# Performance work log

Hardware: AMD Instinct MI355X
Metric: run time of the kernel (lower is better)

Reference implementation:

```python
import jax, jax.numpy as jnp
import numpy as np

B, E, T, H = 4, 16, 1024, 1024
NEG = -10000.0


def setup_inputs() -> dict:
    key = jax.random.key(0)
    ks = jax.random.split(key, 9)
    s = 1.0 / np.sqrt(H)
    return {
        "token_embedding": jax.random.normal(ks[0], (B, T, H), jnp.float32),
        "entity_embedding": jax.random.normal(ks[1], (B, E, H), jnp.float32),
        "token_mask": jax.random.bernoulli(ks[2], 0.9, (B, T)),
        "Wt": jax.random.normal(ks[3], (H, H), jnp.float32) * s,
        "bt": jax.random.normal(ks[4], (H,), jnp.float32) * s,
        "We": jax.random.normal(ks[5], (H, H), jnp.float32) * s,
        "be": jax.random.normal(ks[6], (H,), jnp.float32) * s,
        "Wp": jax.random.normal(ks[7], (H,), jnp.float32) * s,
        "bp": jax.random.normal(ks[8], (1,), jnp.float32) * s,
    }


def reference(token_embedding, entity_embedding, token_mask, Wt, bt, We, be, Wp, bp):
    # token branch: [B,T,H] @ [H,H] -> [B,T,H]
    t = jnp.einsum('bth,hk->btk', token_embedding, Wt) + bt
    # entity branch: [B,E,H] @ [H,H] -> [B,E,H]
    e = jnp.einsum('beh,hk->bek', entity_embedding, We) + be
    # broadcast add -> relu -> linear-to-scalar: [B,E,T,H] -> [B,E,T]
    m = jax.nn.relu(t[:, None, :, :] + e[:, :, None, :])
    cls = jnp.einsum('beth,h->bet', m, Wp) + bp[0]
    # mask fill (after squeeze, per squeeze=True path)
    cls = jnp.where(token_mask[:, None, :], cls, NEG)
    p = jax.nn.sigmoid(cls)
    return cls, p
```

## Files before the change

kernel.cpp:

```cpp
#include <hip/hip_runtime.h>

typedef unsigned short us;
typedef __attribute__((ext_vector_type(8))) short short8;
typedef __attribute__((ext_vector_type(4))) float f32x4;

__device__ __forceinline__ us f2bf(float f) {
  unsigned int u = __builtin_bit_cast(unsigned int, f);
  u += 0x7fffu + ((u >> 16) & 1u);
  return (us)(u >> 16);
}

__device__ __forceinline__ void gload_lds16(const void* g, void* l) {
  __builtin_amdgcn_global_load_lds(
      (const __attribute__((address_space(1))) void*)g,
      (__attribute__((address_space(3))) void*)l, 16, 0, 0);
}

__global__ __launch_bounds__(256) void prep_kernel(
    const float* __restrict__ token, us* __restrict__ tokb,
    const float* __restrict__ Wt, us* __restrict__ WtT,
    const float* __restrict__ entity, const float* __restrict__ We,
    float* __restrict__ epart) {
  __shared__ float tile[64][65];
  __shared__ float eS[16][128];
  const int bid = blockIdx.x, tid = threadIdx.x;
  if (bid < 256) {
    int kc = bid & 7, nt = (bid >> 3) & 7, b = bid >> 6;
    int k0 = kc << 7, n0 = nt << 7;
#pragma unroll
    for (int p = 0; p < 2; ++p) {
      int idx = (p << 8) + tid;
      int r = idx >> 5, kk = (idx & 31) << 2;
      *(float4*)&eS[r][kk] = *(const float4*)&entity[(size_t)(((b << 4) + r) << 10) + k0 + kk];
    }
    __syncthreads();
    const int col = tid & 127, rh = tid >> 7;
    const float* wP = We + ((size_t)k0 << 10) + n0 + col;
    float acc[8] = {0.f, 0.f, 0.f, 0.f, 0.f, 0.f, 0.f, 0.f};
#pragma unroll 8
    for (int k = 0; k < 128; ++k) {
      float wv = wP[(size_t)k << 10];
#pragma unroll
      for (int r = 0; r < 8; ++r)
        acc[r] = fmaf(wv, eS[(rh << 3) + r][k], acc[r]);
    }
    float* op = epart + (((size_t)((kc << 6) + (b << 4) + (rh << 3))) << 10) + n0 + col;
#pragma unroll
    for (int r = 0; r < 8; ++r) op[(size_t)r << 10] = acc[r];
  } else if (bid < 4352) {
    int q = (bid - 256) * 256 + tid;
    float4 v = ((const float4*)token)[q];
    ushort4 o;
    o.x = f2bf(v.x); o.y = f2bf(v.y); o.z = f2bf(v.z); o.w = f2bf(v.w);
    ((ushort4*)tokb)[q] = o;
  } else {
    int tb = bid - 4352;
    int bx = (tb & 15) << 6, by = ((tb >> 4) & 15) << 6;
    int r0 = tid >> 4, c0 = (tid & 15) << 2;
#pragma unroll
    for (int p = 0; p < 4; ++p) {
      int r = p * 16 + r0;
      float4 v = *(const float4*)&Wt[(size_t)(by + r) * 1024 + bx + c0];
      tile[r][c0] = v.x; tile[r][c0 + 1] = v.y;
      tile[r][c0 + 2] = v.z; tile[r][c0 + 3] = v.w;
    }
    __syncthreads();
#pragma unroll
    for (int p = 0; p < 4; ++p) {
      int r = p * 16 + r0;
      ushort4 o;
      o.x = f2bf(tile[c0 + 0][r]); o.y = f2bf(tile[c0 + 1][r]);
      o.z = f2bf(tile[c0 + 2][r]); o.w = f2bf(tile[c0 + 3][r]);
      *(ushort4*)&WtT[(size_t)(bx + r) * 1024 + by + c0] = o;
    }
  }
}

__global__ __launch_bounds__(256) void main_kernel(
    const us* __restrict__ tokb, const us* __restrict__ WtT,
    const float* __restrict__ epart, const float* __restrict__ be,
    const float* __restrict__ bt, const float* __restrict__ wp,
    float* __restrict__ partial) {
  __shared__ __attribute__((aligned(16))) us Ws[2][4096];
  __shared__ __attribute__((aligned(16))) us Ts[2][2048];
  __shared__ __attribute__((aligned(16))) float eL[16][132];
  __shared__ __attribute__((aligned(16))) float btL[128];
  __shared__ __attribute__((aligned(16))) float wpL[128];
  __shared__ float pp[2][64][17];
  const int tid = threadIdx.x;
  const int mh = blockIdx.x, tt = blockIdx.y;
  const int h0 = mh << 7, b = tt >> 4, t0 = (tt & 15) << 6;
#pragma unroll
  for (int p = 0; p < 2; ++p) {
    int q = (p << 8) + tid;
    int er = q >> 5, ec = (q & 31) << 2;
    f32x4 s = *(const f32x4*)&be[h0 + ec];
#pragma unroll
    for (int kc = 0; kc < 8; ++kc)
      s += *(const f32x4*)&epart[(((size_t)((kc << 6) + (b << 4) + er)) << 10) + h0 + ec];
    *(f32x4*)&eL[er][ec] = s;
  }
  if (tid < 128) btL[tid] = bt[h0 + tid];
  else wpL[tid - 128] = wp[h0 + tid - 128];
  asm volatile("" ::: "memory");
  const int row1 = tid >> 2, kc4 = (tid & 3) << 3;
  const us* wP = WtT + (size_t)(h0 + row1) * 1024 + kc4;
  const us* tP = tokb + (size_t)((b << 10) + t0 + row1) * 1024 + kc4;
  const int w = tid >> 6;
  us* w0 = &Ws[0][w * 512]; us* w1 = &Ws[1][w * 512];
  us* t0L = &Ts[0][w * 512]; us* t1L = &Ts[1][w * 512];
  gload_lds16(wP, w0); gload_lds16(wP + 65536, w0 + 2048);
  gload_lds16(tP, t0L);
  gload_lds16(wP + 32, w1); gload_lds16(wP + 65536 + 32, w1 + 2048);
  gload_lds16(tP + 32, t1L);
  const int lane = tid & 63, wm = (tid >> 7) & 1, wn = (tid >> 6) & 1;
  const int l16 = lane & 15, oct = lane >> 4, ko = oct << 3;
  int wfo[4], tfo[2];
#pragma unroll
  for (int i = 0; i < 4; ++i) wfo[i] = (((wm << 6) + (i << 4) + l16) << 5) + ko;
#pragma unroll
  for (int j = 0; j < 2; ++j) tfo[j] = (((wn << 5) + (j << 4) + l16) << 5) + ko;
  f32x4 acc[4][2] = {};
  for (int kt = 0; kt < 32; ++kt) {
    const us* Wb = Ws[kt & 1];
    const us* Tb = Ts[kt & 1];
    __builtin_amdgcn_s_waitcnt(0x0f73);
    __builtin_amdgcn_s_barrier();
    asm volatile("" ::: "memory");
    short8 af[4], bfr[2];
#pragma unroll
    for (int i = 0; i < 4; ++i) af[i] = *(const short8*)&Wb[wfo[i]];
#pragma unroll
    for (int j = 0; j < 2; ++j) bfr[j] = *(const short8*)&Tb[tfo[j]];
#pragma unroll
    for (int i = 0; i < 4; ++i)
#pragma unroll
      for (int j = 0; j < 2; ++j)
        acc[i][j] = __builtin_amdgcn_mfma_f32_16x16x32_bf16(af[i], bfr[j], acc[i][j], 0, 0, 0);
    asm volatile("" ::: "memory");
    __builtin_amdgcn_s_barrier();
    int nk = kt + 2; if (nk > 31) nk = 30;
    int ko2 = nk << 5;
    us* dw = (kt & 1) ? w1 : w0;
    us* dt = (kt & 1) ? t1L : t0L;
    gload_lds16(wP + ko2, dw); gload_lds16(wP + 65536 + ko2, dw + 2048);
    gload_lds16(tP + ko2, dt);
  }
  f32x4 btq[4], wpq[4];
#pragma unroll
  for (int i = 0; i < 4; ++i) {
    int hb = (wm << 6) + (i << 4) + (oct << 2);
    btq[i] = *(const f32x4*)&btL[hb];
    wpq[i] = *(const f32x4*)&wpL[hb];
  }
#pragma unroll
  for (int i = 0; i < 4; ++i)
#pragma unroll
    for (int j = 0; j < 2; ++j) acc[i][j] += btq[i];
#pragma unroll
  for (int e = 0; e < 16; ++e) {
    f32x4 ev[4];
#pragma unroll
    for (int i = 0; i < 4; ++i)
      ev[i] = *(const f32x4*)&eL[e][(wm << 6) + (i << 4) + (oct << 2)];
    float pj[2] = {0.f, 0.f};
#pragma unroll
    for (int j = 0; j < 2; ++j)
#pragma unroll
      for (int i = 0; i < 4; ++i)
#pragma unroll
        for (int r = 0; r < 4; ++r)
          pj[j] = fmaf(fmaxf(acc[i][j][r] + ev[i][r], 0.f), wpq[i][r], pj[j]);
#pragma unroll
    for (int j = 0; j < 2; ++j) {
      pj[j] += __shfl_xor(pj[j], 16, 64);
      pj[j] += __shfl_xor(pj[j], 32, 64);
    }
    if (oct == 0) {
#pragma unroll
      for (int j = 0; j < 2; ++j) pp[wm][(wn << 5) + (j << 4) + l16][e] = pj[j];
    }
  }
  __syncthreads();
#pragma unroll
  for (int q = 0; q < 4; ++q) {
    int flat = (q << 8) + tid;
    int e = flat >> 6, tl = flat & 63;
    float v = pp[0][tl][e] + pp[1][tl][e];
    partial[((size_t)mh << 16) + (size_t)((((b << 4) + e) << 10) + t0 + tl)] = v;
  }
}

__global__ __launch_bounds__(256) void finalize_kernel(
    const float* __restrict__ partial, const float* __restrict__ bp,
    const int* __restrict__ mask, float* __restrict__ out) {
  int idx = blockIdx.x * 256 + threadIdx.x;
  float s = 0.f;
#pragma unroll
  for (int mh = 0; mh < 8; ++mh) s += partial[((size_t)mh << 16) + idx];
  float cls = s + bp[0];
  int b = idx >> 14, t = idx & 1023;
  if (mask[(b << 10) + t] == 0) cls = -10000.0f;
  float p = 1.0f / (1.0f + __expf(-cls));
  out[idx] = cls;
  out[65536 + idx] = p;
}

extern "C" void kernel_launch(void* const* d_in, const int* in_sizes, int n_in,
                              void* d_out, int out_size, void* d_ws, size_t ws_size,
                              hipStream_t stream) {
  const float* token = (const float*)d_in[0];
  const float* entity = (const float*)d_in[1];
  const int* mask = (const int*)d_in[2];
  const float* Wt = (const float*)d_in[3];
  const float* bt = (const float*)d_in[4];
  const float* We = (const float*)d_in[5];
  const float* be = (const float*)d_in[6];
  const float* Wp = (const float*)d_in[7];
  const float* bp = (const float*)d_in[8];
  float* out = (float*)d_out;

  char* ws = (char*)d_ws;
  us* tokb = (us*)ws;
  us* WtT = tokb + (size_t)4096 * 1024;
  float* epart = (float*)(WtT + (size_t)1024 * 1024);
  float* partial = epart + (size_t)8 * 64 * 1024;

  prep_kernel<<<4608, 256, 0, stream>>>(token, tokb, Wt, WtT, entity, We, epart);
  main_kernel<<<dim3(8, 64), 256, 0, stream>>>(tokb, WtT, epart, be, bt, Wp, partial);
  finalize_kernel<<<256, 256, 0, stream>>>(partial, bp, mask, out);
}
```

Measured before the change: 114.2 us.

## Double K-tile depth to 64 and XOR-swizzle LDS layout in main GEMM

The main kernel's K-step per pipeline stage grows from 32 to 64, which halves the number of barrier/wait iterations and issues twice as many MFMAs per sync. The global-to-LDS load mapping is reorganized so each wave loads 8-row by 64-column chunks, with the 16-byte column chunk XOR-swizzled by row to cut LDS bank conflicts on fragment reads. In exchange, LDS usage doubles, which may reduce occupancy, and the waitcnt immediate changes to track six outstanding loads per stage.

```diff
diff --git a/kernel.cpp b/kernel.cpp
--- a/kernel.cpp
+++ b/kernel.cpp
@@ -81,8 +81,8 @@
     const float* __restrict__ epart, const float* __restrict__ be,
     const float* __restrict__ bt, const float* __restrict__ wp,
     float* __restrict__ partial) {
-  __shared__ __attribute__((aligned(16))) us Ws[2][4096];
-  __shared__ __attribute__((aligned(16))) us Ts[2][2048];
+  __shared__ __attribute__((aligned(16))) us Ws[2][8192];
+  __shared__ __attribute__((aligned(16))) us Ts[2][4096];
   __shared__ __attribute__((aligned(16))) float eL[16][132];
   __shared__ __attribute__((aligned(16))) float btL[128];
   __shared__ __attribute__((aligned(16))) float wpL[128];
@@ -103,48 +103,73 @@
   if (tid < 128) btL[tid] = bt[h0 + tid];
   else wpL[tid - 128] = wp[h0 + tid - 128];
   asm volatile("" ::: "memory");
-  const int row1 = tid >> 2, kc4 = (tid & 3) << 3;
-  const us* wP = WtT + (size_t)(h0 + row1) * 1024 + kc4;
-  const us* tP = tokb + (size_t)((b << 10) + t0 + row1) * 1024 + kc4;
-  const int w = tid >> 6;
-  us* w0 = &Ws[0][w * 512]; us* w1 = &Ws[1][w * 512];
-  us* t0L = &Ts[0][w * 512]; us* t1L = &Ts[1][w * 512];
-  gload_lds16(wP, w0); gload_lds16(wP + 65536, w0 + 2048);
-  gload_lds16(tP, t0L);
-  gload_lds16(wP + 32, w1); gload_lds16(wP + 65536 + 32, w1 + 2048);
-  gload_lds16(tP + 32, t1L);
-  const int lane = tid & 63, wm = (tid >> 7) & 1, wn = (tid >> 6) & 1;
-  const int l16 = lane & 15, oct = lane >> 4, ko = oct << 3;
-  int wfo[4], tfo[2];
-#pragma unroll
-  for (int i = 0; i < 4; ++i) wfo[i] = (((wm << 6) + (i << 4) + l16) << 5) + ko;
-#pragma unroll
-  for (int j = 0; j < 2; ++j) tfo[j] = (((wn << 5) + (j << 4) + l16) << 5) + ko;
+  const int w = tid >> 6, lane = tid & 63;
+  const int lr = lane >> 3, lc = lane & 7;
+  const int swz = ((lc ^ lr) << 3);
+  const us* wPs = WtT + (size_t)(h0 + (w << 5) + lr) * 1024 + swz;
+  const us* tPs = tokb + (size_t)((b << 10) + t0 + (w << 4) + lr) * 1024 + swz;
+  us* wD0 = &Ws[0][(w << 5) << 6];
+  us* wD1 = &Ws[1][(w << 5) << 6];
+  us* tD0 = &Ts[0][(w << 4) << 6];
+  us* tD1 = &Ts[1][(w << 4) << 6];
+  auto stage = [&](int kt, us* wD, us* tD) {
+    const us* ws = wPs + (kt << 6);
+    gload_lds16(ws,             wD);
+    gload_lds16(ws + 8 * 1024,  wD + 512);
+    gload_lds16(ws + 16 * 1024, wD + 1024);
+    gload_lds16(ws + 24 * 1024, wD + 1536);
+    const us* ts = tPs + (kt << 6);
+    gload_lds16(ts,            tD);
+    gload_lds16(ts + 8 * 1024, tD + 512);
+  };
+  stage(0, wD0, tD0);
+  stage(1, wD1, tD1);
+  const int l16 = lane & 15, wm = (tid >> 7) & 1, wn = (tid >> 6) & 1, oct = lane >> 4;
+  int wfo[2][4], tfo[2][2];
+#pragma unroll
+  for (int kh = 0; kh < 2; ++kh)
+#pragma unroll
+    for (int i = 0; i < 4; ++i) {
+      int row = (wm << 6) + (i << 4) + l16;
+      wfo[kh][i] = (row << 7) + (((((kh << 2) + oct)) ^ (row & 7)) << 4);
+    }
+#pragma unroll
+  for (int kh = 0; kh < 2; ++kh)
+#pragma unroll
+    for (int j = 0; j < 2; ++j) {
+      int row = (wn << 5) + (j << 4) + l16;
+      tfo[kh][j] = (row << 7) + (((((kh << 2) + oct)) ^ (row & 7)) << 4);
+    }
   f32x4 acc[4][2] = {};
-  for (int kt = 0; kt < 32; ++kt) {
-    const us* Wb = Ws[kt & 1];
-    const us* Tb = Ts[kt & 1];
-    __builtin_amdgcn_s_waitcnt(0x0f73);
+  for (int kt = 0; kt < 16; ++kt) {
+    const char* Wb = (const char*)Ws[kt & 1];
+    const char* Tb = (const char*)Ts[kt & 1];
+    __builtin_amdgcn_s_waitcnt(0x0f76);
     __builtin_amdgcn_s_barrier();
     asm volatile("" ::: "memory");
-    short8 af[4], bfr[2];
-#pragma unroll
-    for (int i = 0; i < 4; ++i) af[i] = *(const short8*)&Wb[wfo[i]];
-#pragma unroll
-    for (int j = 0; j < 2; ++j) bfr[j] = *(const short8*)&Tb[tfo[j]];
+    short8 af[2][4], bfr[2][2];
+#pragma unroll
+    for (int kh = 0; kh < 2; ++kh)
+#pragma unroll
+      for (int i = 0; i < 4; ++i) af[kh][i] = *(const short8*)(Wb + wfo[kh][i]);
+#pragma unroll
+    for (int kh = 0; kh < 2; ++kh)
+#pragma unroll
+      for (int j = 0; j < 2; ++j) bfr[kh][j] = *(const short8*)(Tb + tfo[kh][j]);
 #pragma unroll
     for (int i = 0; i < 4; ++i)
 #pragma unroll
       for (int j = 0; j < 2; ++j)
-        acc[i][j] = __builtin_amdgcn_mfma_f32_16x16x32_bf16(af[i], bfr[j], acc[i][j], 0, 0, 0);
+        acc[i][j] = __builtin_amdgcn_mfma_f32_16x16x32_bf16(af[0][i], bfr[0][j], acc[i][j], 0, 0, 0);
+#pragma unroll
+    for (int i = 0; i < 4; ++i)
+#pragma unroll
+      for (int j = 0; j < 2; ++j)
+        acc[i][j] = __builtin_amdgcn_mfma_f32_16x16x32_bf16(af[1][i], bfr[1][j], acc[i][j], 0, 0, 0);
     asm volatile("" ::: "memory");
     __builtin_amdgcn_s_barrier();
-    int nk = kt + 2; if (nk > 31) nk = 30;
-    int ko2 = nk << 5;
-    us* dw = (kt & 1) ? w1 : w0;
-    us* dt = (kt & 1) ? t1L : t0L;
-    gload_lds16(wP + ko2, dw); gload_lds16(wP + 65536 + ko2, dw + 2048);
-    gload_lds16(tP + ko2, dt);
+    int nk = kt + 2; if (nk > 15) nk = 14;
+    if (kt & 1) stage(nk, wD1, tD1); else stage(nk, wD0, tD0);
   }
   f32x4 btq[4], wpq[4];
 #pragma unroll
```

New measurement: 110.8 us (median of 2 runs). 3.0% less time.
